# Optimization experiments

Hardware: AMD Instinct MI355X
Metric: run time of the kernel (lower is better)

The kernel has to match this reference:

```python
import jax, jax.numpy as jnp
import numpy as np

SIDE = 32
UNITS = SIDE * SIDE  # 1024
BATCH = 128
T = 512


def setup_inputs() -> dict:
    key = jax.random.key(0)
    kx, kb, kb2 = jax.random.split(key, 3)
    # scale inputs so the multiplicative recurrence stays bounded over T steps
    x = jax.random.normal(kx, (BATCH, T, UNITS), dtype=jnp.float32) * 0.05
    # Keras 'uniform' initializer default: U(-0.05, 0.05)
    b = jax.random.uniform(kb, (UNITS,), jnp.float32, -0.05, 0.05)
    b2 = jax.random.uniform(kb2, (UNITS,), jnp.float32, -0.05, 0.05)
    h0 = jnp.zeros((BATCH, UNITS), dtype=jnp.float32)
    return {"x": x, "b": b, "b2": b2, "h0": h0}


def reference(x, b, b2, h0):
    """MinimalRNNCell unrolled over time via lax.scan.

    Per step: out = reshape( (b2 + h) as [B,s,s] @ (b + x_t) as [B,s,s] , [B, s*s])
    Returns the last hidden state [B, UNITS] (Keras RNN return_sequences=False).
    """
    Bsz = x.shape[0]

    def step(h, x_t):
        A = (b2 + h).reshape(Bsz, SIDE, SIDE)      # [B,s,s]
        M = (b + x_t).reshape(Bsz, SIDE, SIDE)     # [B,s,s]
        out = jnp.einsum('bij,bjk->bik', A, M).reshape(Bsz, UNITS)
        return out, None

    x_tbu = jnp.swapaxes(x, 0, 1)  # [T, B, UNITS]
    h_last, _ = jax.lax.scan(step, h0, x_tbu)
    return h_last
```

## Files before the change

### kernel.cpp

```cpp
#include <hip/hip_runtime.h>

#define TSTEPS 512
#define NP 7
#define S  32

typedef __bf16 bf16x8 __attribute__((ext_vector_type(8)));
typedef float f32x16 __attribute__((ext_vector_type(16)));
typedef unsigned int uint4v __attribute__((ext_vector_type(4)));

#if __has_builtin(__builtin_amdgcn_cvt_pk_bf16_f32)
__device__ __forceinline__ unsigned packbf(float lo, float hi) {
    return __builtin_bit_cast(unsigned, __builtin_amdgcn_cvt_pk_bf16_f32(lo, hi));
}
#else
__device__ __forceinline__ unsigned rne_(float f) {
    unsigned u = __float_as_uint(f);
    return u + 0x7fffu + ((u >> 16) & 1u);
}
__device__ __forceinline__ unsigned packbf(float lo, float hi) {
    return __builtin_amdgcn_perm(rne_(hi), rne_(lo), 0x07060302u);
}
#endif

__device__ __forceinline__ int ldf(const int* p) {
    return __hip_atomic_load(p, __ATOMIC_RELAXED, __HIP_MEMORY_SCOPE_WORKGROUP);
}
__device__ __forceinline__ void stf(int* p, int v) {
    __hip_atomic_store(p, v, __ATOMIC_RELAXED, __HIP_MEMORY_SCOPE_WORKGROUP);
}

__global__ void __launch_bounds__(64 * (NP + 1), 1)
minrnn_kernel(const float* __restrict__ x, const float* __restrict__ bvec,
              const float* __restrict__ b2vec, const float* __restrict__ h0,
              float* __restrict__ out)
{
    __shared__ unsigned ring[S * 512];
    __shared__ int flags[S];
    __shared__ int consumed;

    const int tid  = threadIdx.x;
    const int wave = tid >> 6;
    const int l    = tid & 63;
    const int col  = l & 31;
    const int half = l >> 5;
    const int bb   = blockIdx.x;

    if (tid < S) flags[tid] = 0;
    if (tid == 0) consumed = -1;
    __syncthreads();

    if (wave == 0) {
        float u[16];
        f32x16 cb2;
#pragma unroll
        for (int i = 0; i < 16; ++i) {
            const int row = (i & 3) + 8 * (i >> 2) + 4 * half;
            const float b2v = b2vec[col * 32 + row];
            cb2[i] = b2v;
            u[i] = h0[bb * 1024 + col * 32 + row] + b2v;
        }

        int flagn = ldf(&flags[0]);
        while (flagn != 1) flagn = ldf(&flags[0]);
        __threadfence_block();
        unsigned cur[8], nxt[8];
#pragma unroll
        for (int d = 0; d < 8; ++d) cur[d] = ring[d * 64 + l];
        flagn = ldf(&flags[1]);

        for (int t = 0; t < TSTEPS; ++t) {
            if (t < TSTEPS - 1) {
                const int want = t + 2;
                while (flagn != want) flagn = ldf(&flags[(t + 1) & (S - 1)]);
                __threadfence_block();
                const int sb = ((t + 1) & (S - 1)) << 9;
#pragma unroll
                for (int d = 0; d < 8; ++d) nxt[d] = ring[sb + d * 64 + l];
                if (t + 2 < TSTEPS) flagn = ldf(&flags[(t + 2) & (S - 1)]);
            }

            unsigned pb[8];
#pragma unroll
            for (int i = 0; i < 8; ++i) pb[i] = packbf(u[2 * i], u[2 * i + 1]);
            const bf16x8 B0 = __builtin_bit_cast(bf16x8, (uint4v){pb[0], pb[1], pb[2], pb[3]});
            const bf16x8 B1 = __builtin_bit_cast(bf16x8, (uint4v){pb[4], pb[5], pb[6], pb[7]});
            const bf16x8 A0 = __builtin_bit_cast(bf16x8, (uint4v){cur[0], cur[1], cur[2], cur[3]});
            const bf16x8 A1 = __builtin_bit_cast(bf16x8, (uint4v){cur[4], cur[5], cur[6], cur[7]});

            f32x16 acc = __builtin_amdgcn_mfma_f32_32x32x16_bf16(A0, B0, cb2, 0, 0, 0);
            acc        = __builtin_amdgcn_mfma_f32_32x32x16_bf16(A1, B1, acc, 0, 0, 0);
#pragma unroll
            for (int i = 0; i < 16; ++i) u[i] = acc[i];

            if (l == 0 && (t & 7) == 7) stf(&consumed, t);
#pragma unroll
            for (int d = 0; d < 8; ++d) cur[d] = nxt[d];
        }

#pragma unroll
        for (int i = 0; i < 16; ++i) {
            const int row = (i & 3) + 8 * (i >> 2) + 4 * half;
            out[bb * 1024 + col * 32 + row] = u[i] - cb2[i];
        }
    } else {
        const int p = wave - 1;
        float bA[16];
        int off[16];
#pragma unroll
        for (int c = 0; c < 2; ++c)
#pragma unroll
            for (int j = 0; j < 8; ++j) {
                const int k = c * 16 + half * 4 + (j & 3) + 8 * (j >> 2);
                bA[c * 8 + j] = bvec[k * 32 + col];
                off[c * 8 + j] = c * 512 + half * 128 + (j >> 2) * 256 + (j & 3) * 32 + col;
            }
        const float* xb = x + (size_t)bb * TSTEPS * 1024;

        auto emit = [&](int t, const float* v) {
            while (ldf(&consumed) < t - 33) {}
            unsigned pa[8];
#pragma unroll
            for (int i = 0; i < 8; ++i)
                pa[i] = packbf(v[2 * i] + bA[2 * i], v[2 * i + 1] + bA[2 * i + 1]);
            const int sb = (t & (S - 1)) << 9;
#pragma unroll
            for (int d = 0; d < 8; ++d) ring[sb + d * 64 + l] = pa[d];
            __threadfence_block();
            if (l == 0) stf(&flags[t & (S - 1)], t + 1);
        };

        for (int t = p; t < TSTEPS; t += 2 * NP) {
            const int t2 = t + NP;
            float va[16], vb[16];
#pragma unroll
            for (int i = 0; i < 16; ++i) va[i] = xb[t * 1024 + off[i]];
            if (t2 < TSTEPS) {
#pragma unroll
                for (int i = 0; i < 16; ++i) vb[i] = xb[t2 * 1024 + off[i]];
            }
            __builtin_amdgcn_sched_barrier(0);
            emit(t, va);
            if (t2 < TSTEPS) emit(t2, vb);
        }
    }
}

extern "C" void kernel_launch(void* const* d_in, const int* in_sizes, int n_in,
                              void* d_out, int out_size, void* d_ws, size_t ws_size,
                              hipStream_t stream)
{
    const float* x  = (const float*)d_in[0];
    const float* b  = (const float*)d_in[1];
    const float* b2 = (const float*)d_in[2];
    const float* h0 = (const float*)d_in[3];
    float* out = (float*)d_out;
    minrnn_kernel<<<128, 64 * (NP + 1), 0, stream>>>(x, b, b2, h0, out);
}
```

Measured before the change: 364.8 us.

## Add helper blocks that prefetch x into cache ahead of the recurrence

Launches a second set of 128 blocks that stream each batch's x slice a bounded distance ahead of the compute block's progress, which is published through a workspace counter. The helpers sum the values into a sink so the loads are not optimised away. The aim is to have x resident in L2/MALL before the producer waves read it, hiding HBM latency on the serial path. The cost is extra memory traffic, cross-block polling, and reliance on the workspace never being initialised (a garbage counter is clamped to zero).

```diff
diff --git a/kernel.cpp b/kernel.cpp
--- a/kernel.cpp
+++ b/kernel.cpp
@@ -3,6 +3,8 @@
 #define TSTEPS 512
 #define NP 7
 #define S  32
+#define NCB 128
+#define LEAD 40
 
 typedef __bf16 bf16x8 __attribute__((ext_vector_type(8)));
 typedef float f32x16 __attribute__((ext_vector_type(16)));
@@ -32,8 +34,36 @@
 __global__ void __launch_bounds__(64 * (NP + 1), 1)
 minrnn_kernel(const float* __restrict__ x, const float* __restrict__ bvec,
               const float* __restrict__ b2vec, const float* __restrict__ h0,
-              float* __restrict__ out)
+              float* __restrict__ out, int* __restrict__ prog)
 {
+    const int bid = blockIdx.x;
+
+    if (bid >= NCB) {
+        const int bb   = bid - NCB;
+        const int wave = threadIdx.x >> 6;
+        const int l    = threadIdx.x & 63;
+        const float4* xb = (const float4*)(x + (size_t)bb * TSTEPS * 1024);
+        float4 acc = {0.f, 0.f, 0.f, 0.f};
+        int pg = 0;
+        for (int t = wave; t < TSTEPS; t += 8) {
+            while (t > pg + LEAD) {
+                int p = __hip_atomic_load(&prog[bb], __ATOMIC_RELAXED,
+                                          __HIP_MEMORY_SCOPE_AGENT);
+                pg = (p < 0 || p > TSTEPS) ? 0 : p;
+                if (t <= pg + LEAD) break;
+                __builtin_amdgcn_s_sleep(8);
+            }
+#pragma unroll
+            for (int q = 0; q < 4; ++q) {
+                float4 v = xb[t * 256 + q * 64 + l];
+                acc.x += v.x; acc.y += v.y; acc.z += v.z; acc.w += v.w;
+            }
+        }
+        float* sink = (float*)(prog + 256);
+        sink[(size_t)bid * 512 + threadIdx.x] = acc.x + acc.y + acc.z + acc.w;
+        return;
+    }
+
     __shared__ unsigned ring[S * 512];
     __shared__ int flags[S];
     __shared__ int consumed;
@@ -43,7 +73,7 @@
     const int l    = tid & 63;
     const int col  = l & 31;
     const int half = l >> 5;
-    const int bb   = blockIdx.x;
+    const int bb   = bid;
 
     if (tid < S) flags[tid] = 0;
     if (tid == 0) consumed = -1;
@@ -92,7 +122,12 @@
 #pragma unroll
             for (int i = 0; i < 16; ++i) u[i] = acc[i];
 
-            if (l == 0 && (t & 7) == 7) stf(&consumed, t);
+            if (l == 0) {
+                if ((t & 7) == 7) stf(&consumed, t);
+                if ((t & 15) == 15)
+                    __hip_atomic_store(&prog[bb], t, __ATOMIC_RELAXED,
+                                       __HIP_MEMORY_SCOPE_AGENT);
+            }
 #pragma unroll
             for (int d = 0; d < 8; ++d) cur[d] = nxt[d];
         }
@@ -154,5 +189,6 @@
     const float* b2 = (const float*)d_in[2];
     const float* h0 = (const float*)d_in[3];
     float* out = (float*)d_out;
-    minrnn_kernel<<<128, 64 * (NP + 1), 0, stream>>>(x, b, b2, h0, out);
+    int* prog = (int*)d_ws;
+    minrnn_kernel<<<2 * NCB, 64 * (NP + 1), 0, stream>>>(x, b, b2, h0, out, prog);
 }
```

New measurement: 397.9 us. +9.1%, slower.
